# Kernel tuning notes

Hardware: AMD Instinct MI355X
Metric: run time of the kernel (lower is better)

Reference implementation:

```python
import jax, jax.numpy as jnp
import numpy as np

N_NODES = 100000
N_EDGES = 1600000
D_H = 64
D_E = 64
D_Q = 64
D_HID = 128
N_GRAPHS = 16


def _mlp_params(key, d_in, d_hid):
    k1, k2, k3, k4 = jax.random.split(key, 4)
    s1 = 1.0 / np.sqrt(d_in)
    s2 = 1.0 / np.sqrt(d_hid)
    return (
        jax.random.uniform(k1, (d_in, d_hid), jnp.float32, -s1, s1),
        jax.random.uniform(k2, (d_hid,), jnp.float32, -s1, s1),
        jax.random.uniform(k3, (d_hid, 1), jnp.float32, -s2, s2),
        jax.random.uniform(k4, (1,), jnp.float32, -s2, s2),
    )


def setup_inputs() -> dict:
    key = jax.random.key(0)
    ks = jax.random.split(key, 8)
    h = jax.random.normal(ks[0], (N_NODES, D_H), jnp.float32)
    e = jax.random.normal(ks[1], (N_EDGES, D_E), jnp.float32)
    q = jax.random.normal(ks[2], (N_GRAPHS, D_Q), jnp.float32)
    edge_index = jax.random.randint(ks[3], (2, N_EDGES), 0, N_NODES, jnp.int64)
    edge_batch = jax.random.randint(ks[4], (N_EDGES,), 0, N_GRAPHS, jnp.int64)
    gw1, gb1, gw2, gb2 = _mlp_params(ks[5], 2 * D_H + D_Q, D_HID)
    sw1, sb1, sw2, sb2 = _mlp_params(ks[6], 2 * D_H + D_E, D_HID)
    return {
        "h": h, "e": e, "q": q,
        "edge_index": edge_index, "edge_batch": edge_batch,
        "gate_w1": gw1, "gate_b1": gb1, "gate_w2": gw2, "gate_b2": gb2,
        "score_w1": sw1, "score_b1": sb1, "score_w2": sw2, "score_b2": sb2,
    }


def _mlp(x, w1, b1, w2, b2):
    # 2-layer MLP, no layernorm (use_layer_norm=False), output dim 1
    hidden = jax.nn.relu(x @ w1 + b1)
    return (hidden @ w2 + b2)[..., 0]


def _dst_softmax(raw, dst, num_nodes):
    # numerically stable per-destination softmax via segment reductions
    max_vals = jax.ops.segment_max(raw, dst, num_segments=num_nodes)
    exp_vals = jnp.exp(raw - max_vals[dst])
    sum_exp = jax.ops.segment_sum(exp_vals, dst, num_segments=num_nodes)
    denom = jnp.maximum(sum_exp[dst], 1e-9)
    return exp_vals / denom


def reference(h, e, q, edge_index, edge_batch,
              gate_w1, gate_b1, gate_w2, gate_b2,
              score_w1, score_b1, score_w2, score_b2):
    src, dst = edge_index[0], edge_index[1]
    h_i = h[src]            # [E, d_h]
    h_j = h[dst]            # [E, d_h]
    q_e = q[edge_batch]     # [E, d_q]
    gate_in = jnp.concatenate([h_i, h_j, q_e], axis=-1)
    gate = jax.nn.sigmoid(_mlp(gate_in, gate_w1, gate_b1, gate_w2, gate_b2))
    score_in = jnp.concatenate([h_i, h_j, e], axis=-1)
    score = _mlp(score_in, score_w1, score_b1, score_w2, score_b2)
    raw = gate * score
    return _dst_softmax(raw, dst, h.shape[0])
```

## Files before the change

### kernel.cpp

```cpp
#include <hip/hip_runtime.h>
#include <hip/hip_bf16.h>

#define NN 100000
#define NE 1600000

typedef __attribute__((ext_vector_type(8))) unsigned short ushort8v;
typedef __attribute__((ext_vector_type(4))) unsigned short ushort4v;
typedef __attribute__((ext_vector_type(8))) short short8v;
typedef __attribute__((ext_vector_type(4))) float f32x4;

__device__ __forceinline__ float b2f(unsigned short u) {
  return __uint_as_float(((unsigned)u) << 16);
}
__device__ __forceinline__ short f2bs(float f) {
  unsigned u = __float_as_uint(f);
  unsigned r = (u + 0x7FFFu + ((u >> 16) & 1u)) >> 16;
  return (short)r;
}

__global__ void qproj_kernel(const float* __restrict__ q,
                             const float* __restrict__ gw1,
                             const float* __restrict__ gb1,
                             float* __restrict__ Qg) {
  int g = blockIdx.x, j = threadIdx.x;
  float acc = gb1[j];
  for (int k = 0; k < 64; ++k) acc += q[g * 64 + k] * gw1[(128 + k) * 128 + j];
  Qg[g * 128 + j] = acc;
}

__global__ __launch_bounds__(1024) void prepack_kernel(
    const float* __restrict__ sw1, short8v* __restrict__ WtG) {
  int tid = threadIdx.x;
  int t = tid >> 7, ks = (tid >> 6) & 1, lane = tid & 63;
  int qg = lane >> 4, cl = lane & 15;
  short8v fr;
#pragma unroll
  for (int j = 0; j < 8; ++j)
    fr[j] = f2bs(sw1[(128 + ks * 32 + qg * 8 + j) * 128 + t * 16 + cl]);
  WtG[tid] = fr;
}

__global__ __launch_bounds__(256) void nodeproj_kernel(
    const float* __restrict__ h, const float* __restrict__ gw1,
    const float* __restrict__ sw1, __hip_bfloat16* __restrict__ GA,
    __hip_bfloat16* __restrict__ GB, __hip_bfloat16* __restrict__ SA,
    __hip_bfloat16* __restrict__ SB) {
  __shared__ float hs[64][64];
  __shared__ float Ws[64][128];
  int part = blockIdx.y;
  const float* W = (part & 1) ? sw1 : gw1;
  int roff = (part >= 2) ? 64 : 0;
  __hip_bfloat16* outp = (part == 0) ? GA : (part == 1) ? SA : (part == 2) ? GB : SB;
  int n0 = blockIdx.x * 64;
  int t = threadIdx.x;

  {
    int n = t & 63, kc = t >> 6;
    int gn = n0 + n;
#pragma unroll
    for (int i = 0; i < 4; ++i) {
      int k = kc * 16 + i * 4;
      float4 hv = make_float4(0.f, 0.f, 0.f, 0.f);
      if (gn < NN) hv = *(const float4*)&h[gn * 64 + k];
      hs[k + 0][n] = hv.x; hs[k + 1][n] = hv.y;
      hs[k + 2][n] = hv.z; hs[k + 3][n] = hv.w;
    }
  }
  {
    const float* Wb = W + roff * 128;
    float* wsf = &Ws[0][0];
#pragma unroll
    for (int i = 0; i < 8; ++i) {
      int flat = (i * 256 + t) * 4;
      *(float4*)&wsf[flat] = *(const float4*)&Wb[flat];
    }
  }
  __syncthreads();

  int tx = t & 31, ty = t >> 5;
  float acc[8][4] = {};
#pragma unroll 4
  for (int k = 0; k < 64; ++k) {
    float hn[8];
    *(float4*)&hn[0] = *(const float4*)&hs[k][ty * 8];
    *(float4*)&hn[4] = *(const float4*)&hs[k][ty * 8 + 4];
    float wv[4];
#pragma unroll
    for (int i = 0; i < 4; ++i) wv[i] = Ws[k][tx + 32 * i];
#pragma unroll
    for (int j = 0; j < 8; ++j)
#pragma unroll
      for (int i = 0; i < 4; ++i) acc[j][i] += hn[j] * wv[i];
  }
#pragma unroll
  for (int j = 0; j < 8; ++j) {
    int gn = n0 + ty * 8 + j;
    if (gn < NN) {
#pragma unroll
      for (int i = 0; i < 4; ++i)
        outp[(size_t)gn * 128 + tx + 32 * i] = __float2bfloat16(acc[j][i]);
    }
  }
}

__global__ __launch_bounds__(256) void edge_kernel(
    const float* __restrict__ e, const int* __restrict__ eidx,
    const int* __restrict__ ebat,
    const __hip_bfloat16* __restrict__ GA, const __hip_bfloat16* __restrict__ GB,
    const __hip_bfloat16* __restrict__ SA, const __hip_bfloat16* __restrict__ SB,
    const float* __restrict__ Qg, const short8v* __restrict__ WtG,
    const float* __restrict__ sb1, const float* __restrict__ gw2,
    const float* __restrict__ gb2, const float* __restrict__ sw2,
    const float* __restrict__ sb2, float* __restrict__ out,
    float* __restrict__ nsum) {
  __shared__ short8v WtS[1024];
  __shared__ f32x4 QgS[512];
  __shared__ f32x4 gw2S[32], sb1S[32], sw2S[32];
  const int tid = threadIdx.x;
  const int w = tid >> 6, lane = tid & 63;
  const int qg = lane >> 4, cl = lane & 15;
  const int EB = blockIdx.x * 256 + w * 64;
  const unsigned short* GAU = (const unsigned short*)GA;
  const unsigned short* GBU = (const unsigned short*)GB;
  const unsigned short* SAU = (const unsigned short*)SA;
  const unsigned short* SBU = (const unsigned short*)SB;
  const float sb2v = sb2[0], gb2v = gb2[0];

  {
    const f32x4* s4 = (const f32x4*)WtG;
    f32x4* d4 = (f32x4*)WtS;
#pragma unroll
    for (int i = 0; i < 4; ++i) d4[tid + i * 256] = s4[tid + i * 256];
    const f32x4* q4 = (const f32x4*)Qg;
    QgS[tid] = q4[tid];
    QgS[tid + 256] = q4[tid + 256];
    if (tid < 32) {
      gw2S[tid] = ((const f32x4*)gw2)[tid];
      sb1S[tid] = ((const f32x4*)sb1)[tid];
      sw2S[tid] = ((const f32x4*)sw2)[tid];
    }
  }
  __syncthreads();

#pragma unroll 1
  for (int rt = 0; rt < 4; ++rt) {
    const int erow = EB + rt * 16 + cl;
    const int srcv = eidx[erow];
    const int dstv = eidx[NE + erow];
    const int g = ebat[erow];

    const float* ap = e + (size_t)erow * 64 + qg * 8;
    f32x4 f0 = __builtin_nontemporal_load((const f32x4*)(ap + 0));
    f32x4 f1 = __builtin_nontemporal_load((const f32x4*)(ap + 4));
    f32x4 f2 = __builtin_nontemporal_load((const f32x4*)(ap + 32));
    f32x4 f3 = __builtin_nontemporal_load((const f32x4*)(ap + 36));

    const unsigned short* sr = SAU + (size_t)srcv * 128 + qg * 4;
    const unsigned short* dr = SBU + (size_t)dstv * 128 + qg * 4;
    const unsigned short* gr = GAU + (size_t)srcv * 128 + qg * 4;
    const unsigned short* hr = GBU + (size_t)dstv * 128 + qg * 4;
    ushort4v sav[8], sbv[8], gav[8], gbv[8];
#pragma unroll
    for (int t = 0; t < 8; ++t) {
      sav[t] = *(const ushort4v*)(sr + t * 16);
      sbv[t] = *(const ushort4v*)(dr + t * 16);
      gav[t] = *(const ushort4v*)(gr + t * 16);
      gbv[t] = *(const ushort4v*)(hr + t * 16);
    }

    short8v b0, b1;
    b0[0] = f2bs(f0.x); b0[1] = f2bs(f0.y); b0[2] = f2bs(f0.z); b0[3] = f2bs(f0.w);
    b0[4] = f2bs(f1.x); b0[5] = f2bs(f1.y); b0[6] = f2bs(f1.z); b0[7] = f2bs(f1.w);
    b1[0] = f2bs(f2.x); b1[1] = f2bs(f2.y); b1[2] = f2bs(f2.z); b1[3] = f2bs(f2.w);
    b1[4] = f2bs(f3.x); b1[5] = f2bs(f3.y); b1[6] = f2bs(f3.z); b1[7] = f2bs(f3.w);

    float part = 0.f, gpart = 0.f;
#pragma unroll
    for (int t = 0; t < 8; ++t) {
      short8v Aw0 = WtS[(t * 2 + 0) * 64 + lane];
      short8v Aw1 = WtS[(t * 2 + 1) * 64 + lane];
      f32x4 acc = (f32x4){0.f, 0.f, 0.f, 0.f};
      acc = __builtin_amdgcn_mfma_f32_16x16x32_bf16(Aw0, b0, acc, 0, 0, 0);
      acc = __builtin_amdgcn_mfma_f32_16x16x32_bf16(Aw1, b1, acc, 0, 0, 0);
      f32x4 bb = sb1S[t * 4 + qg];
      f32x4 ww = sw2S[t * 4 + qg];
      f32x4 qv = QgS[g * 32 + t * 4 + qg];
      f32x4 g2 = gw2S[t * 4 + qg];
#pragma unroll
      for (int i = 0; i < 4; ++i) {
        float sx = acc[i] + b2f(sav[t][i]) + b2f(sbv[t][i]) + bb[i];
        part = fmaf(fmaxf(sx, 0.f), ww[i], part);
        float gx = b2f(gav[t][i]) + b2f(gbv[t][i]) + qv[i];
        gpart = fmaf(fmaxf(gx, 0.f), g2[i], gpart);
      }
    }
    part += __shfl_xor(part, 16, 64);
    part += __shfl_xor(part, 32, 64);
    gpart += __shfl_xor(gpart, 16, 64);
    gpart += __shfl_xor(gpart, 32, 64);
    if (lane < 16) {
      int E = EB + rt * 16 + cl;
      float gate = 1.f / (1.f + __expf(-(gpart + gb2v)));
      float ex = __expf(gate * (part + sb2v));
      out[E] = ex;
      atomicAdd(&nsum[dstv], ex);
    }
  }
}

__global__ __launch_bounds__(256) void norm_kernel(
    const int* __restrict__ eidx, const float* __restrict__ nodesum,
    float* __restrict__ out) {
  int ee = blockIdx.x * 256 + threadIdx.x;
  int dst = eidx[NE + ee];
  out[ee] = out[ee] / fmaxf(nodesum[dst], 1e-9f);
}

extern "C" void kernel_launch(void* const* d_in, const int* in_sizes, int n_in,
                              void* d_out, int out_size, void* d_ws, size_t ws_size,
                              hipStream_t stream) {
  const float* h   = (const float*)d_in[0];
  const float* e   = (const float*)d_in[1];
  const float* q   = (const float*)d_in[2];
  const int* eidx  = (const int*)d_in[3];
  const int* ebat  = (const int*)d_in[4];
  const float* gw1 = (const float*)d_in[5];
  const float* gb1 = (const float*)d_in[6];
  const float* gw2 = (const float*)d_in[7];
  const float* gb2 = (const float*)d_in[8];
  const float* sw1 = (const float*)d_in[9];
  const float* sb1 = (const float*)d_in[10];
  const float* sw2 = (const float*)d_in[11];
  const float* sb2 = (const float*)d_in[12];
  float* out = (float*)d_out;

  char* ws = (char*)d_ws;
  __hip_bfloat16* GA = (__hip_bfloat16*)ws;
  __hip_bfloat16* GB = (__hip_bfloat16*)(ws + 25600000);
  __hip_bfloat16* SA = (__hip_bfloat16*)(ws + 51200000);
  __hip_bfloat16* SB = (__hip_bfloat16*)(ws + 76800000);
  float* Qg    = (float*)(ws + 102400000);
  short8v* WtG = (short8v*)(ws + 102400000 + 8192);
  float* nsum  = (float*)(ws + 102400000 + 8192 + 16384);

  (void)hipMemsetAsync(nsum, 0, 400000, stream);
  qproj_kernel<<<dim3(16), dim3(128), 0, stream>>>(q, gw1, gb1, Qg);
  prepack_kernel<<<dim3(1), dim3(1024), 0, stream>>>(sw1, WtG);
  nodeproj_kernel<<<dim3(1563, 4), dim3(256), 0, stream>>>(h, gw1, sw1, GA, GB, SA, SB);
  edge_kernel<<<dim3(NE / 256), dim3(256), 0, stream>>>(
      e, eidx, ebat, GA, GB, SA, SB, Qg, WtG, sb1, gw2, gb2, sw2, sb2, out, nsum);
  norm_kernel<<<dim3(NE / 256), dim3(256), 0, stream>>>(eidx, nsum, out);
}
```

Measured before the change: 605.7 us.

## Prefetch edge indices, vectorize gate gathers, pad Qg shared layout

Each wave now loads the next row-tile's src/dst/batch indices during the current iteration, so the index load no longer sits on the dependent gather's critical path. The gate-projection gathers switch from eight 8-byte loads to four 16-byte contiguous loads per lane, with the gate dot product reorganized over contiguous hidden units. The shared Qg table is padded to a stride of 33 to reduce LDS bank conflicts. Costs are extra registers for the prefetched indices and wider gather vectors, which may lower occupancy.

New measurement: 529.8 us. 1.14x faster.

```diff
diff --git a/kernel.cpp b/kernel.cpp
--- a/kernel.cpp
+++ b/kernel.cpp
@@ -114,7 +114,7 @@
     const float* __restrict__ sb2, float* __restrict__ out,
     float* __restrict__ nsum) {
   __shared__ short8v WtS[1024];
-  __shared__ f32x4 QgS[512];
+  __shared__ f32x4 QgS[16 * 33];
   __shared__ f32x4 gw2S[32], sb1S[32], sw2S[32];
   const int tid = threadIdx.x;
   const int w = tid >> 6, lane = tid & 63;
@@ -126,14 +126,21 @@
   const unsigned short* SBU = (const unsigned short*)SB;
   const float sb2v = sb2[0], gb2v = gb2[0];
 
+  int srcv = eidx[EB + cl];
+  int dstv = eidx[NE + EB + cl];
+  int gv   = ebat[EB + cl];
+
   {
     const f32x4* s4 = (const f32x4*)WtG;
     f32x4* d4 = (f32x4*)WtS;
 #pragma unroll
     for (int i = 0; i < 4; ++i) d4[tid + i * 256] = s4[tid + i * 256];
     const f32x4* q4 = (const f32x4*)Qg;
-    QgS[tid] = q4[tid];
-    QgS[tid + 256] = q4[tid + 256];
+    QgS[(tid >> 5) * 33 + (tid & 31)] = q4[tid];
+    {
+      int t2 = tid + 256;
+      QgS[(t2 >> 5) * 33 + (t2 & 31)] = q4[t2];
+    }
     if (tid < 32) {
       gw2S[tid] = ((const f32x4*)gw2)[tid];
       sb1S[tid] = ((const f32x4*)sb1)[tid];
@@ -145,9 +152,6 @@
 #pragma unroll 1
   for (int rt = 0; rt < 4; ++rt) {
     const int erow = EB + rt * 16 + cl;
-    const int srcv = eidx[erow];
-    const int dstv = eidx[NE + erow];
-    const int g = ebat[erow];
 
     const float* ap = e + (size_t)erow * 64 + qg * 8;
     f32x4 f0 = __builtin_nontemporal_load((const f32x4*)(ap + 0));
@@ -155,17 +159,29 @@
     f32x4 f2 = __builtin_nontemporal_load((const f32x4*)(ap + 32));
     f32x4 f3 = __builtin_nontemporal_load((const f32x4*)(ap + 36));
 
+    const unsigned short* gr = GAU + (size_t)srcv * 128 + qg * 32;
+    const unsigned short* hr = GBU + (size_t)dstv * 128 + qg * 32;
+    ushort8v gav[4], gbv[4];
+#pragma unroll
+    for (int c = 0; c < 4; ++c) {
+      gav[c] = *(const ushort8v*)(gr + c * 8);
+      gbv[c] = *(const ushort8v*)(hr + c * 8);
+    }
     const unsigned short* sr = SAU + (size_t)srcv * 128 + qg * 4;
     const unsigned short* dr = SBU + (size_t)dstv * 128 + qg * 4;
-    const unsigned short* gr = GAU + (size_t)srcv * 128 + qg * 4;
-    const unsigned short* hr = GBU + (size_t)dstv * 128 + qg * 4;
-    ushort4v sav[8], sbv[8], gav[8], gbv[8];
+    ushort4v sav[8], sbv[8];
 #pragma unroll
     for (int t = 0; t < 8; ++t) {
       sav[t] = *(const ushort4v*)(sr + t * 16);
       sbv[t] = *(const ushort4v*)(dr + t * 16);
-      gav[t] = *(const ushort4v*)(gr + t * 16);
-      gbv[t] = *(const ushort4v*)(hr + t * 16);
+    }
+
+    int srcn = srcv, dstn = dstv, gn = gv;
+    if (rt < 3) {
+      int er2 = erow + 16;
+      srcn = eidx[er2];
+      dstn = eidx[NE + er2];
+      gn   = ebat[er2];
     }
 
     short8v b0, b1;
@@ -174,7 +190,27 @@
     b1[0] = f2bs(f2.x); b1[1] = f2bs(f2.y); b1[2] = f2bs(f2.z); b1[3] = f2bs(f2.w);
     b1[4] = f2bs(f3.x); b1[5] = f2bs(f3.y); b1[6] = f2bs(f3.z); b1[7] = f2bs(f3.w);
 
-    float part = 0.f, gpart = 0.f;
+    float gpart = 0.f;
+#pragma unroll
+    for (int c = 0; c < 4; ++c) {
+      ushort8v av = gav[c], bv = gbv[c];
+      f32x4 q0 = QgS[gv * 33 + qg * 8 + c * 2];
+      f32x4 q1 = QgS[gv * 33 + qg * 8 + c * 2 + 1];
+      f32x4 w0 = gw2S[qg * 8 + c * 2];
+      f32x4 w1 = gw2S[qg * 8 + c * 2 + 1];
+#pragma unroll
+      for (int ii = 0; ii < 4; ++ii) {
+        float x = b2f(av[ii]) + b2f(bv[ii]) + q0[ii];
+        gpart = fmaf(fmaxf(x, 0.f), w0[ii], gpart);
+      }
+#pragma unroll
+      for (int ii = 0; ii < 4; ++ii) {
+        float x = b2f(av[4 + ii]) + b2f(bv[4 + ii]) + q1[ii];
+        gpart = fmaf(fmaxf(x, 0.f), w1[ii], gpart);
+      }
+    }
+
+    float part = 0.f;
 #pragma unroll
     for (int t = 0; t < 8; ++t) {
       short8v Aw0 = WtS[(t * 2 + 0) * 64 + lane];
@@ -184,16 +220,13 @@
       acc = __builtin_amdgcn_mfma_f32_16x16x32_bf16(Aw1, b1, acc, 0, 0, 0);
       f32x4 bb = sb1S[t * 4 + qg];
       f32x4 ww = sw2S[t * 4 + qg];
-      f32x4 qv = QgS[g * 32 + t * 4 + qg];
-      f32x4 g2 = gw2S[t * 4 + qg];
 #pragma unroll
       for (int i = 0; i < 4; ++i) {
         float sx = acc[i] + b2f(sav[t][i]) + b2f(sbv[t][i]) + bb[i];
         part = fmaf(fmaxf(sx, 0.f), ww[i], part);
-        float gx = b2f(gav[t][i]) + b2f(gbv[t][i]) + qv[i];
-        gpart = fmaf(fmaxf(gx, 0.f), g2[i], gpart);
       }
     }
+
     part += __shfl_xor(part, 16, 64);
     part += __shfl_xor(part, 32, 64);
     gpart += __shfl_xor(gpart, 16, 64);
@@ -205,6 +238,7 @@
       out[E] = ex;
       atomicAdd(&nsum[dstv], ex);
     }
+    srcv = srcn; dstv = dstn; gv = gn;
   }
 }
 
```
